# Kernel optimization log

Measured on AMD Instinct MI355X. Metric: run time of the kernel, lower is better.

Reference implementation:

```python
import jax, jax.numpy as jnp
import numpy as np

DIM = 512
HEADS = 8
HD = DIM // HEADS

def _rotate_half(t):
    t1, t2 = jnp.split(t, 2, axis=-1)
    return jnp.concatenate((-t2, t1), axis=-1)

def _layernorm(x, g, b, eps=1e-5):
    mu = jnp.mean(x, axis=-1, keepdims=True)
    var = jnp.var(x, axis=-1, keepdims=True)
    return (x - mu) * jax.lax.rsqrt(var + eps) * g + b

def setup_inputs() -> dict:
    key = jax.random.key(0)
    ks = jax.random.split(key, 12)
    B, S = 4, 2048
    x = jax.random.normal(ks[0], (B, S, DIM), dtype=jnp.float32)
    rope_cos = jax.random.uniform(ks[1], (1, S, 1, HD), dtype=jnp.float32)
    rope_sin = jax.random.uniform(ks[2], (1, S, 1, HD), dtype=jnp.float32)
    sd = 1.0 / np.sqrt(DIM)
    params = {
        'norm1_g': jnp.ones((DIM,), jnp.float32),
        'norm1_b': jnp.zeros((DIM,), jnp.float32),
        'norm2_g': jnp.ones((DIM,), jnp.float32),
        'norm2_b': jnp.zeros((DIM,), jnp.float32),
        'w_qkv': jax.random.uniform(ks[3], (DIM, 3 * DIM), jnp.float32, -sd, sd),
        'b_qkv': jax.random.uniform(ks[4], (3 * DIM,), jnp.float32, -sd, sd),
        'w_proj': jax.random.uniform(ks[5], (DIM, DIM), jnp.float32, -sd, sd),
        'b_proj': jax.random.uniform(ks[6], (DIM,), jnp.float32, -sd, sd),
        'w_fc1': jax.random.uniform(ks[7], (DIM, 4 * DIM), jnp.float32, -sd, sd),
        'b_fc1': jax.random.uniform(ks[8], (4 * DIM,), jnp.float32, -sd, sd),
        'w_fc2': jax.random.uniform(ks[9], (4 * DIM, DIM), jnp.float32, -1.0 / np.sqrt(4 * DIM), 1.0 / np.sqrt(4 * DIM)),
        'b_fc2': jax.random.uniform(ks[10], (DIM,), jnp.float32, -1.0 / np.sqrt(4 * DIM), 1.0 / np.sqrt(4 * DIM)),
    }
    return {'x': x, 'rope_cos': rope_cos, 'rope_sin': rope_sin, **params}

def reference(x, rope_cos, rope_sin, norm1_g, norm1_b, norm2_g, norm2_b,
              w_qkv, b_qkv, w_proj, b_proj, w_fc1, b_fc1, w_fc2, b_fc2):
    B, S, D = x.shape
    scale = 1.0 / np.sqrt(HD)
    shortcut = x
    h = _layernorm(x, norm1_g, norm1_b)
    qkv = (h @ w_qkv + b_qkv).reshape(B, S, 3, HEADS, HD)
    q, k, v = qkv[:, :, 0], qkv[:, :, 1], qkv[:, :, 2]  # [B,S,H,hd]
    q = q * rope_cos + _rotate_half(q) * rope_sin
    k = k * rope_cos + _rotate_half(k) * rope_sin
    # attention over heads: scores [B,H,S,S]
    attn = jnp.einsum('bqhd,bkhd->bhqk', q, k) * scale
    attn = jax.nn.softmax(attn, axis=-1)
    o = jnp.einsum('bhqk,bkhd->bqhd', attn, v).reshape(B, S, D)
    o = o @ w_proj + b_proj
    x = shortcut + o  # dropout is identity in eval
    h2 = _layernorm(x, norm2_g, norm2_b)
    mlp = jax.nn.gelu(h2 @ w_fc1 + b_fc1, approximate=False) @ w_fc2 + b_fc2
    return x + mlp
```

## Files before the change

### kernel.cpp

```cpp
#include <hip/hip_runtime.h>
#include <cstdint>
#include <cstddef>

typedef unsigned short u16;
typedef unsigned int   u32;
typedef __bf16 bf16x8 __attribute__((ext_vector_type(8)));
typedef float  f32x4  __attribute__((ext_vector_type(4)));

#define BS   8192
#define DIMM 512
#define NH   8
#define HD   64
#define SEQ  2048
#define DFF  2048
#define NQKV 1536

#define GLD16(g, l) __builtin_amdgcn_global_load_lds( \
    (__attribute__((address_space(1))) const void*)(g), \
    (__attribute__((address_space(3))) void*)(l), 16, 0, 0)

__device__ __forceinline__ float b2f(u16 s) {
  u32 u = ((u32)s) << 16;
  float f; __builtin_memcpy(&f, &u, 4); return f;
}
__device__ __forceinline__ u16 f2b(float f) {
  u32 u; __builtin_memcpy(&u, &f, 4);
  u += 0x7fffu + ((u >> 16) & 1u);
  return (u16)(u >> 16);
}
__device__ __forceinline__ u16 f2b_rtz(float f) {
  u32 u; __builtin_memcpy(&u, &f, 4);
  return (u16)(u >> 16);
}

#define SZ_QKV (DIMM * NQKV)
#define SZ_PRJ (DIMM * DIMM)
#define SZ_F1  (DIMM * DFF)
#define SZ_F2  (DFF * DIMM)
__global__ __launch_bounds__(256) void transpose_all_k(
    const float* __restrict__ w_qkv, const float* __restrict__ w_prj,
    const float* __restrict__ w_f1,  const float* __restrict__ w_f2,
    u16* __restrict__ o_qkv, u16* __restrict__ o_prj,
    u16* __restrict__ o_f1,  u16* __restrict__ o_f2) {
  int idx = blockIdx.x * 256 + threadIdx.x;
  const float* W; u16* O; int Kd, Nd, off;
  if (idx < SZ_QKV)                         { W = w_qkv; O = o_qkv; Kd = DIMM; Nd = NQKV; off = idx; }
  else if (idx < SZ_QKV + SZ_PRJ)           { W = w_prj; O = o_prj; Kd = DIMM; Nd = DIMM; off = idx - SZ_QKV; }
  else if (idx < SZ_QKV + SZ_PRJ + SZ_F1)   { W = w_f1;  O = o_f1;  Kd = DIMM; Nd = DFF;  off = idx - SZ_QKV - SZ_PRJ; }
  else                                      { W = w_f2;  O = o_f2;  Kd = DFF;  Nd = DIMM; off = idx - SZ_QKV - SZ_PRJ - SZ_F1; }
  int n = off / Kd, k = off - n * Kd;
  O[off] = f2b(W[(size_t)k * Nd + n]);
}

__global__ __launch_bounds__(256) void ln_f32b_k(const float* __restrict__ X,
    const float* __restrict__ G, const float* __restrict__ Bb, u16* __restrict__ out) {
  int w = threadIdx.x >> 6, lane = threadIdx.x & 63;
  size_t row = (size_t)blockIdx.x * 4 + w;
  const float* xr = X + row * DIMM;
  float v[8];
  *(float4*)&v[0] = *(const float4*)(xr + lane * 8);
  *(float4*)&v[4] = *(const float4*)(xr + lane * 8 + 4);
  float s = 0.f, s2 = 0.f;
#pragma unroll
  for (int j = 0; j < 8; j++) { s += v[j]; s2 += v[j] * v[j]; }
#pragma unroll
  for (int m = 1; m < 64; m <<= 1) { s += __shfl_xor(s, m); s2 += __shfl_xor(s2, m); }
  float mu = s * (1.f / DIMM);
  float rsd = rsqrtf(s2 * (1.f / DIMM) - mu * mu + 1e-5f);
  float g[8], bb[8];
  *(float4*)&g[0]  = *(const float4*)(G + lane * 8);
  *(float4*)&g[4]  = *(const float4*)(G + lane * 8 + 4);
  *(float4*)&bb[0] = *(const float4*)(Bb + lane * 8);
  *(float4*)&bb[4] = *(const float4*)(Bb + lane * 8 + 4);
  uint4 ov; u16* os = (u16*)&ov;
#pragma unroll
  for (int j = 0; j < 8; j++) os[j] = f2b((v[j] - mu) * rsd * g[j] + bb[j]);
  *(uint4*)(out + row * DIMM + lane * 8) = ov;
}

template <int EPI, int TM, int TN, int BK>
__global__ __launch_bounds__(256) void gemm_bt(const u16* __restrict__ A,
    const u16* __restrict__ BT, const float* __restrict__ bias,
    void* __restrict__ Cout, const float* __restrict__ resid, int N, int Kd) {
  constexpr int CPR  = BK / 8;
  constexpr int CPRB = (BK == 64) ? 3 : 2;
  constexpr int RS   = (BK == 64) ? 0 : 1;
  constexpr int KK   = BK / 32;
  constexpr int WROWS = (TN == 128) ? TM / 2 : TM / 4;
  constexpr int MT   = WROWS / 16;
  constexpr int ALOOP = TM * CPR / 256;
  constexpr int BLOOP = TN * CPR / 256;
  __shared__ __align__(16) u16 a_s[2][TM * BK];
  __shared__ __align__(16) u16 b_s[2][TN * BK];
  int t = threadIdx.x, lane = t & 63, w = t >> 6;
  int l15 = lane & 15, quad = lane >> 4;
  int gx = gridDim.x;
  int lid = blockIdx.x + gx * blockIdx.y;
  int per = (gx * gridDim.y) >> 3;
  int nid = (lid & 7) * per + (lid >> 3);
  int bx = nid % gx, by = nid / gx;
  int m0 = by * TM, n0 = bx * TN;
  int wm = (TN == 128) ? (w >> 1) * WROWS : w * WROWS;
  int wn = (TN == 128) ? (w & 1) * 64 : 0;
  f32x4 z4 = {0.f, 0.f, 0.f, 0.f};
  f32x4 acc[MT][4];
#pragma unroll
  for (int i = 0; i < MT; i++)
#pragma unroll
    for (int j = 0; j < 4; j++) acc[i][j] = z4;

#define GSTAGE(buf, ts) do {                                                  \
    int k0_ = (ts) * BK;                                                      \
    _Pragma("unroll")                                                         \
    for (int i = 0; i < ALOOP; i++) {                                         \
      int c_ = t + i * 256;                                                   \
      int row_ = c_ >> CPRB, pos_ = c_ & (CPR - 1);                           \
      int ch_ = (pos_ ^ (row_ >> RS)) & (CPR - 1);                            \
      GLD16(A + (size_t)(m0 + row_) * Kd + k0_ + ch_ * 8, &a_s[buf][c_ * 8]); \
    }                                                                         \
    _Pragma("unroll")                                                         \
    for (int i = 0; i < BLOOP; i++) {                                         \
      int c_ = t + i * 256;                                                   \
      int row_ = c_ >> CPRB, pos_ = c_ & (CPR - 1);                           \
      int ch_ = (pos_ ^ (row_ >> RS)) & (CPR - 1);                            \
      GLD16(BT + (size_t)(n0 + row_) * Kd + k0_ + ch_ * 8, &b_s[buf][c_ * 8]);\
    }                                                                         \
  } while (0)

#define GCOMPUTE(buf) do {                                                    \
    bf16x8 af[MT][KK], bfm[4][KK];                                            \
    _Pragma("unroll")                                                         \
    for (int mt = 0; mt < MT; mt++) {                                         \
      _Pragma("unroll")                                                       \
      for (int kk = 0; kk < KK; kk++) {                                       \
        int row_ = wm + mt * 16 + l15;                                        \
        int pos_ = ((kk * 4 + quad) ^ (row_ >> RS)) & (CPR - 1);              \
        af[mt][kk] = *(const bf16x8*)&a_s[buf][row_ * BK + pos_ * 8];         \
      }                                                                       \
    }                                                                         \
    _Pragma("unroll")                                                         \
    for (int nt = 0; nt < 4; nt++) {                                          \
      _Pragma("unroll")                                                       \
      for (int kk = 0; kk < KK; kk++) {                                       \
        int row_ = wn + nt * 16 + l15;                                        \
        int pos_ = ((kk * 4 + quad) ^ (row_ >> RS)) & (CPR - 1);              \
        bfm[nt][kk] = *(const bf16x8*)&b_s[buf][row_ * BK + pos_ * 8];        \
      }                                                                       \
    }                                                                         \
    _Pragma("unroll")                                                         \
    for (int kk = 0; kk < KK; kk++)                                           \
      _Pragma("unroll")                                                       \
      for (int mt = 0; mt < MT; mt++)                                         \
        _Pragma("unroll")                                                     \
        for (int nt = 0; nt < 4; nt++)                                        \
          acc[mt][nt] = __builtin_amdgcn_mfma_f32_16x16x32_bf16(              \
              af[mt][kk], bfm[nt][kk], acc[mt][nt], 0, 0, 0);                 \
  } while (0)

  GSTAGE(0, 0);
  __syncthreads();
  int nsteps = Kd / BK;
  for (int ts = 0; ts < nsteps; ts += 2) {
    GSTAGE(1, ts + 1);
    GCOMPUTE(0);
    __syncthreads();
    if (ts + 2 < nsteps) GSTAGE(0, ts + 2);
    GCOMPUTE(1);
    __syncthreads();
  }
#undef GSTAGE
#undef GCOMPUTE

#pragma unroll
  for (int nt = 0; nt < 4; nt++) {
    int col = n0 + wn + nt * 16 + l15;
    float bv = bias[col];
#pragma unroll
    for (int mt = 0; mt < MT; mt++) {
#pragma unroll
      for (int r = 0; r < 4; r++) {
        int rw = m0 + wm + mt * 16 + quad * 4 + r;
        float v = acc[mt][nt][r] + bv;
        size_t off = (size_t)rw * N + col;
        if (EPI == 0) {
          ((float*)Cout)[off] = v;
        } else if (EPI == 1) {
          ((float*)Cout)[off] = v + resid[off];
        } else if (EPI == 2) {
          ((u16*)Cout)[off] = f2b(0.5f * v * (1.f + erff(v * 0.70710678118654752f)));
        } else {
          ((u16*)Cout)[off] = f2b(v);
        }
      }
    }
  }
}

#define QSCALE 0.18033688f
__global__ __launch_bounds__(256) void rope_k(const u16* __restrict__ qkv,
    const float* __restrict__ C, const float* __restrict__ Sn,
    u16* __restrict__ Qo, u16* __restrict__ Ko, u16* __restrict__ Vo) {
  int idx = blockIdx.x * 256 + threadIdx.x;
  int row = idx / 192;
  int cn = idx - row * 192;
  int n0 = cn * 8;
  int comp = n0 >> 9;
  int hh = (n0 >> 6) & 7;
  int d0 = n0 & 63;
  int b = row >> 11, s = row & 2047;
  const u16* src = qkv + (size_t)row * NQKV;
  uint4 val = *(const uint4*)(src + n0);
  u16* vs = (u16*)&val;
  size_t oo = ((size_t)((b << 3) + hh) * SEQ + s) * HD + d0;
  if (comp == 2) { *(uint4*)(Vo + oo) = val; return; }
  uint4 pv = *(const uint4*)(src + (n0 ^ 32));
  u16* ps = (u16*)&pv;
  float cv[8], sv[8];
  *(float4*)&cv[0] = *(const float4*)(C + s * HD + d0);
  *(float4*)&cv[4] = *(const float4*)(C + s * HD + d0 + 4);
  *(float4*)&sv[0] = *(const float4*)(Sn + s * HD + d0);
  *(float4*)&sv[4] = *(const float4*)(Sn + s * HD + d0 + 4);
  float sgn = (d0 & 32) ? 1.f : -1.f;
  float sc = (comp == 0) ? QSCALE : 1.f;
  uint4 ov; u16* os = (u16*)&ov;
#pragma unroll
  for (int j = 0; j < 8; j++)
    os[j] = f2b(sc * (b2f(vs[j]) * cv[j] + sgn * b2f(ps[j]) * sv[j]));
  *(uint4*)((comp == 0 ? Qo : Ko) + oo) = ov;
}

__global__ __launch_bounds__(256) void vtrans_k(const u16* __restrict__ V,
                                                u16* __restrict__ Vt) {
  __shared__ u16 ld[64 * 72];
  int t = threadIdx.x;
  int bh = blockIdx.x >> 5;
  int s0 = (blockIdx.x & 31) * 64;
  const u16* src = V + (size_t)bh * SEQ * HD + (size_t)s0 * HD;
  u16* dst = Vt + (size_t)bh * SEQ * HD;
#pragma unroll
  for (int i = 0; i < 2; i++) {
    int c = t + i * 256, s = c >> 3, cp = c & 7;
    *(uint4*)&ld[s * 72 + ((cp ^ (s >> 3)) << 3)] =
        *(const uint4*)(src + (size_t)s * HD + cp * 8);
  }
  __syncthreads();
#pragma unroll
  for (int i = 0; i < 2; i++) {
    int c = t + i * 256, d = c >> 3, sc = c & 7;
    uint4 ov; u16* os = (u16*)&ov;
#pragma unroll
    for (int j = 0; j < 8; j++) {
      int s = sc * 8 + j;
      os[j] = ld[s * 72 + (((d >> 3) ^ (s >> 3)) << 3) + (d & 7)];
    }
    *(uint4*)(dst + (size_t)d * SEQ + s0 + sc * 8) = ov;
  }
}

__global__ __launch_bounds__(512) void attn_flash_k(const u16* __restrict__ Qg,
    const u16* __restrict__ Kg, const u16* __restrict__ Vtg, u16* __restrict__ Og) {
  __shared__ u16 q_s[128 * 72];
  __shared__ u16 k_s[64 * 72];
  __shared__ u16 vt_s[64 * 72];
  int t = threadIdx.x, lane = t & 63, w = t >> 6;
  int l15 = lane & 15, quad = lane >> 4;
  int lid = blockIdx.x;
  int nid = (lid & 7) * 64 + (lid >> 3);
  int bh = nid >> 4;
  int qt0 = (nid & 15) * 128;
  int b = bh >> 3, h = bh & 7;
  const u16* Qp = Qg + (size_t)bh * SEQ * HD;
  const u16* Kp = Kg + (size_t)bh * SEQ * HD;
  const u16* Vp = Vtg + (size_t)bh * SEQ * HD;
  int row = t >> 3, ch = t & 7;

  int sW = (w * 4 + quad) & 7;
  int pcol[4];
#pragma unroll
  for (int n = 0; n < 4; n++)
    pcol[n] = (((n * 2 + (l15 >> 3)) ^ sW) << 3) + (l15 & 7);
  int sR = (w * 4 + (l15 >> 2)) & 7;
  int pch[2];
#pragma unroll
  for (int kk = 0; kk < 2; kk++)
    pch[kk] = ((kk * 4 + quad) ^ sR) << 3;

#pragma unroll
  for (int i = 0; i < 2; i++) {
    int c = t + i * 512, qr = c >> 3, qc = c & 7;
    *(uint4*)&q_s[qr * 72 + qc * 8] = *(const uint4*)(Qp + (size_t)(qt0 + qr) * HD + qc * 8);
  }
  uint4 kr = *(const uint4*)(Kp + (size_t)row * HD + ch * 8);
  uint4 vr = *(const uint4*)(Vp + (size_t)row * SEQ + ch * 8);
  __syncthreads();
  bf16x8 qa[2];
  qa[0] = *(const bf16x8*)&q_s[(w * 16 + l15) * 72 + quad * 8];
  qa[1] = *(const bf16x8*)&q_s[(w * 16 + l15) * 72 + 32 + quad * 8];
  u16* p_s = q_s;
  f32x4 z4 = {0.f, 0.f, 0.f, 0.f};
  f32x4 of[4];
#pragma unroll
  for (int n = 0; n < 4; n++) of[n] = z4;
  float lrun[4] = {};

  for (int kt = 0; kt < SEQ; kt += 64) {
    __syncthreads();
    *(uint4*)&k_s[row * 72 + ch * 8] = kr;
    *(uint4*)&vt_s[row * 72 + ch * 8] = vr;
    __syncthreads();
    if (kt + 64 < SEQ) {
      kr = *(const uint4*)(Kp + (size_t)(kt + 64 + row) * HD + ch * 8);
      vr = *(const uint4*)(Vp + (size_t)row * SEQ + kt + 64 + ch * 8);
    }
    f32x4 sf[4];
#pragma unroll
    for (int n = 0; n < 4; n++) sf[n] = z4;
    __builtin_amdgcn_s_setprio(1);
#pragma unroll
    for (int kk = 0; kk < 2; kk++)
#pragma unroll
      for (int n = 0; n < 4; n++) {
        bf16x8 kb = *(const bf16x8*)&k_s[(n * 16 + l15) * 72 + kk * 32 + quad * 8];
        sf[n] = __builtin_amdgcn_mfma_f32_16x16x32_bf16(qa[kk], kb, sf[n], 0, 0, 0);
      }
    __builtin_amdgcn_s_setprio(0);
#pragma unroll
    for (int r = 0; r < 4; r++) {
      int prow = (w * 16 + quad * 4 + r) * 72;
#pragma unroll
      for (int n = 0; n < 4; n++) {
        float pp = exp2f(sf[n][r]);
        lrun[r] += pp;
        p_s[prow + pcol[n]] = f2b_rtz(pp);
      }
    }
    __builtin_amdgcn_s_setprio(1);
#pragma unroll
    for (int kk = 0; kk < 2; kk++) {
      bf16x8 pa = *(const bf16x8*)&p_s[(w * 16 + l15) * 72 + pch[kk]];
#pragma unroll
      for (int n = 0; n < 4; n++) {
        bf16x8 vb = *(const bf16x8*)&vt_s[(n * 16 + l15) * 72 + kk * 32 + quad * 8];
        of[n] = __builtin_amdgcn_mfma_f32_16x16x32_bf16(pa, vb, of[n], 0, 0, 0);
      }
    }
    __builtin_amdgcn_s_setprio(0);
  }
#pragma unroll
  for (int r = 0; r < 4; r++) {
    float l = lrun[r];
#pragma unroll
    for (int m = 1; m < 16; m <<= 1) l += __shfl_xor(l, m);
    float inv = 1.f / l;
    size_t orow = (size_t)(b * SEQ + qt0 + w * 16 + quad * 4 + r);
#pragma unroll
    for (int n = 0; n < 4; n++)
      Og[orow * DIMM + h * HD + n * 16 + l15] = f2b(of[n][r] * inv);
  }
}

extern "C" void kernel_launch(void* const* d_in, const int* in_sizes, int n_in,
                              void* d_out, int out_size, void* d_ws, size_t ws_size,
                              hipStream_t stream) {
  const float* x    = (const float*)d_in[0];
  const float* rc   = (const float*)d_in[1];
  const float* rsn  = (const float*)d_in[2];
  const float* n1g  = (const float*)d_in[3];
  const float* n1b  = (const float*)d_in[4];
  const float* n2g  = (const float*)d_in[5];
  const float* n2b  = (const float*)d_in[6];
  const float* wqkv = (const float*)d_in[7];
  const float* bqkv = (const float*)d_in[8];
  const float* wprj = (const float*)d_in[9];
  const float* bprj = (const float*)d_in[10];
  const float* wf1  = (const float*)d_in[11];
  const float* bf1  = (const float*)d_in[12];
  const float* wf2  = (const float*)d_in[13];
  const float* bf2  = (const float*)d_in[14];

  char* p = (char*)d_ws;
  u16*   wqkvT = (u16*)p;
  u16*   wprjT = (u16*)(p + (2u  << 20));
  u16*   wf1T  = (u16*)(p + (3u  << 20));
  u16*   wf2T  = (u16*)(p + (5u  << 20));
  u16*   h1    = (u16*)(p + (8u  << 20));
  u16*   qkvb  = (u16*)(p + (16u << 20));
  u16*   Vt    = (u16*)(p + (40u << 20));
  u16*   Qb    = (u16*)(p + (64u << 20));
  u16*   Kb    = (u16*)(p + (72u << 20));
  u16*   Vb    = (u16*)(p + (80u << 20));
  float* x2    = (float*)(p + (88u << 20));
  u16*   ob    = h1;
  u16*   h2    = h1;
  u16*   mid   = qkvb;

  transpose_all_k<<<dim3((SZ_QKV + SZ_PRJ + SZ_F1 + SZ_F2) / 256), 256, 0, stream>>>(
      wqkv, wprj, wf1, wf2, wqkvT, wprjT, wf1T, wf2T);

  ln_f32b_k<<<dim3(BS / 4), 256, 0, stream>>>(x, n1g, n1b, h1);

  gemm_bt<3, 128, 128, 32><<<dim3(NQKV / 128, BS / 128), 256, 0, stream>>>(h1, wqkvT, bqkv, qkvb, nullptr, NQKV, DIMM);

  rope_k<<<dim3(BS * NQKV / 8 / 256), 256, 0, stream>>>(qkvb, rc, rsn, Qb, Kb, Vb);

  vtrans_k<<<dim3(32 * (SEQ / 64)), 256, 0, stream>>>(Vb, Vt);

  attn_flash_k<<<dim3(32 * (SEQ / 128)), 512, 0, stream>>>(Qb, Kb, Vt, ob);

  gemm_bt<1, 64, 64, 64><<<dim3(DIMM / 64, BS / 64), 256, 0, stream>>>(ob, wprjT, bprj, x2, x, DIMM, DIMM);

  ln_f32b_k<<<dim3(BS / 4), 256, 0, stream>>>(x2, n2g, n2b, h2);

  gemm_bt<2, 128, 128, 32><<<dim3(DFF / 128, BS / 128), 256, 0, stream>>>(h2, wf1T, bf1, mid, nullptr, DFF, DIMM);

  gemm_bt<1, 64, 64, 64><<<dim3(DIMM / 64, BS / 64), 256, 0, stream>>>(mid, wf2T, bf2, (float*)d_out, x2, DIMM, DFF);
}
```

Before: 305.8 us.

## Restructure GEMM double-buffer pipeline with explicit vmcnt waits and split frag/MFMA

Splits the GEMM compute step into separate LDS fragment loads and MFMA issue. The main loop now keeps two global-to-LDS stages in flight, using explicit s_waitcnt vmcnt and lgkmcnt plus raw barriers in place of __syncthreads. Prefetching the next stage while the MFMAs run is meant to hide more global load latency. The hardcoded vmcnt(4) assumes a specific number of outstanding loads per stage, which risks being wrong for some template instantiations.

```diff
diff --git a/kernel.cpp b/kernel.cpp
--- a/kernel.cpp
+++ b/kernel.cpp
@@ -18,6 +18,11 @@
 #define GLD16(g, l) __builtin_amdgcn_global_load_lds( \
     (__attribute__((address_space(1))) const void*)(g), \
     (__attribute__((address_space(3))) void*)(l), 16, 0, 0)
+
+#define SBAR   __builtin_amdgcn_s_barrier()
+#define VMCNT4 asm volatile("s_waitcnt vmcnt(4)" ::: "memory")
+#define VMCNT0 asm volatile("s_waitcnt vmcnt(0)" ::: "memory")
+#define LGKM0  asm volatile("s_waitcnt lgkmcnt(0)" ::: "memory")
 
 __device__ __forceinline__ float b2f(u16 s) {
   u32 u = ((u32)s) << 16;
@@ -127,8 +132,7 @@
     }                                                                         \
   } while (0)
 
-#define GCOMPUTE(buf) do {                                                    \
-    bf16x8 af[MT][KK], bfm[4][KK];                                            \
+#define GFRAG(buf) do {                                                       \
     _Pragma("unroll")                                                         \
     for (int mt = 0; mt < MT; mt++) {                                         \
       _Pragma("unroll")                                                       \
@@ -147,6 +151,9 @@
         bfm[nt][kk] = *(const bf16x8*)&b_s[buf][row_ * BK + pos_ * 8];        \
       }                                                                       \
     }                                                                         \
+  } while (0)
+
+#define GMFMA() do {                                                          \
     _Pragma("unroll")                                                         \
     for (int kk = 0; kk < KK; kk++)                                           \
       _Pragma("unroll")                                                       \
@@ -157,19 +164,41 @@
               af[mt][kk], bfm[nt][kk], acc[mt][nt], 0, 0, 0);                 \
   } while (0)
 
+  bf16x8 af[MT][KK], bfm[4][KK];
   GSTAGE(0, 0);
-  __syncthreads();
+  GSTAGE(1, 1);
+  VMCNT4;
+  SBAR;
   int nsteps = Kd / BK;
   for (int ts = 0; ts < nsteps; ts += 2) {
-    GSTAGE(1, ts + 1);
-    GCOMPUTE(0);
-    __syncthreads();
-    if (ts + 2 < nsteps) GSTAGE(0, ts + 2);
-    GCOMPUTE(1);
-    __syncthreads();
+    GFRAG(0);
+    LGKM0;
+    SBAR;
+    if (ts + 2 < nsteps) {
+      GSTAGE(0, ts + 2);
+      GMFMA();
+      VMCNT4;
+    } else {
+      GMFMA();
+      VMCNT0;
+    }
+    SBAR;
+    GFRAG(1);
+    LGKM0;
+    SBAR;
+    if (ts + 3 < nsteps) {
+      GSTAGE(1, ts + 3);
+      GMFMA();
+      VMCNT4;
+    } else {
+      GMFMA();
+      VMCNT0;
+    }
+    SBAR;
   }
 #undef GSTAGE
-#undef GCOMPUTE
+#undef GFRAG
+#undef GMFMA
 
 #pragma unroll
   for (int nt = 0; nt < 4; nt++) {
```

Result: slower. 340.4 us (+11.3%).
